# Optimization experiments

Hardware: AMD Instinct MI355X
Metric: run time of the kernel (lower is better)

The kernel has to match this reference:

```python
import jax, jax.numpy as jnp
import numpy as np

NUM_HEADS = 16
LN_EPS = 1e-5

def _gelu(x):
    return jax.nn.gelu(x, approximate=False)  # torch default GELU is exact (erf)

def setup_inputs() -> dict:
    key = jax.random.key(0)
    ks = jax.random.split(key, 12)
    B, S, E = 2, 2048, 1024
    H = E // 2
    s = lambda fan_in: 1.0 / np.sqrt(fan_in)
    inp = {
        "x": jax.random.normal(ks[0], (B, S, E), jnp.float32),
        "Wq": jax.random.normal(ks[1], (E, E), jnp.float32) * s(E),
        "bq": jnp.zeros((E,), jnp.float32),
        "Wk": jax.random.normal(ks[2], (E, E), jnp.float32) * s(E),
        "bk": jnp.zeros((E,), jnp.float32),
        "Wv": jax.random.normal(ks[3], (E, E), jnp.float32) * s(E),
        "bv": jnp.zeros((E,), jnp.float32),
        "Wo": jax.random.normal(ks[4], (E, E), jnp.float32) * s(E),
        "bo": jnp.zeros((E,), jnp.float32),
        "dp_w1": jax.random.normal(ks[5], (E, H), jnp.float32) * s(E),
        "dp_b1": jnp.zeros((H,), jnp.float32),
        "ln_g": jnp.ones((H,), jnp.float32),
        "ln_b": jnp.zeros((H,), jnp.float32),
        "dp_w2": jax.random.normal(ks[6], (H, 1), jnp.float32) * s(H),
        "dp_b2": jnp.zeros((1,), jnp.float32),
        "g_w1": jax.random.normal(ks[7], (1, 16), jnp.float32),
        "g_b1": jnp.zeros((16,), jnp.float32),
        "g_w2": jax.random.normal(ks[8], (16, 1), jnp.float32) * s(16),
        "g_b2": jnp.zeros((1,), jnp.float32),
    }
    return inp


def reference(x, Wq, bq, Wk, bk, Wv, bv, Wo, bo,
              dp_w1, dp_b1, ln_g, ln_b, dp_w2, dp_b2,
              g_w1, g_b1, g_w2, g_b2):
    B, S, E = x.shape
    Hn = NUM_HEADS
    Dh = E // Hn
    scale = Dh ** -0.5

    Q = (x @ Wq + bq).reshape(B, S, Hn, Dh)
    K = (x @ Wk + bk).reshape(B, S, Hn, Dh)
    V = (x @ Wv + bv).reshape(B, S, Hn, Dh)

    # (B, H, q, k)
    logits = jnp.einsum('bqhd,bkhd->bhqk', Q, K) * scale
    causal = jnp.tril(jnp.ones((S, S), bool))
    logits = jnp.where(causal, logits, -jnp.inf)
    attn = jax.nn.softmax(logits, axis=-1)

    # drift probe: Linear -> LayerNorm -> GELU -> Linear, squeeze -> (B, S)
    h = x @ dp_w1 + dp_b1
    mu = h.mean(-1, keepdims=True)
    var = ((h - mu) ** 2).mean(-1, keepdims=True)
    h = (h - mu) / jnp.sqrt(var + LN_EPS) * ln_g + ln_b
    drift = (_gelu(h) @ dp_w2 + dp_b2)[..., 0]

    # drift_to_gate: Linear(1,16) -> GELU -> Linear(16,1) -> Tanh -> (B, S)
    g = _gelu(drift[..., None] * g_w1[0] + g_b1)
    gate = jnp.tanh(g @ g_w2 + g_b2)[..., 0]  # (B, S), indexed by key position

    gated = attn * gate[:, None, None, :]  # dropout p=0 -> identity
    out = jnp.einsum('bhqk,bkhd->bqhd', gated, V).reshape(B, S, E)
    return out @ Wo + bo
```

## Files before the change

### kernel.cpp

```cpp
#include <hip/hip_runtime.h>
#include <math.h>
#include <stdint.h>

#define B_   2
#define S_   2048
#define E_   1024
#define NH   16
#define DH   64
#define HID  512
#define NCAT 3584
#define MTOK 4096

typedef unsigned short ushort_t;
typedef short  s16x8  __attribute__((ext_vector_type(8)));
typedef unsigned short us4 __attribute__((ext_vector_type(4)));
typedef float  f32x4  __attribute__((ext_vector_type(4)));

static constexpr float LN_EPS    = 1e-5f;
static constexpr float SCALE     = 0.125f;
static constexpr float INV_SQRT2 = 0.70710678118654752440f;

__device__ __forceinline__ float gelu_exact(float v) {
    return 0.5f * v * (1.0f + erff(v * INV_SQRT2));
}

__device__ __forceinline__ ushort_t f2bf(float f) {
    unsigned int u = __float_as_uint(f);
    unsigned int r = u + 0x7fffu + ((u >> 16) & 1u);
    return (ushort_t)(r >> 16);
}
__device__ __forceinline__ float bf2f(ushort_t s) {
    return __uint_as_float(((unsigned int)s) << 16);
}

__device__ __forceinline__ void stage16(const void* g, void* ldsbase) {
#if __has_builtin(__builtin_amdgcn_global_load_lds)
    __builtin_amdgcn_global_load_lds(
        (const __attribute__((address_space(1))) void*)g,
        (__attribute__((address_space(3))) void*)ldsbase, 16, 0, 0);
#else
    ((uint4*)ldsbase)[threadIdx.x & 63] = *(const uint4*)g;
#endif
}

__device__ __forceinline__ void xcd_swizzle(int gx, int gy, int& bx, int& by) {
    const int T = gx * gy;
    const int lin = blockIdx.y * gx + blockIdx.x;
    const int work = (lin & 7) * (T >> 3) + (lin >> 3);
    bx = work % gx;
    by = work / gx;
}

__global__ __launch_bounds__(256) void split_kernel(
    const float* __restrict__ src, ushort_t* __restrict__ dh,
    ushort_t* __restrict__ dl, int n4)
{
    int i = blockIdx.x * 256 + threadIdx.x;
    if (i >= n4) return;
    float4 v = ((const float4*)src)[i];
    float vv[4] = {v.x, v.y, v.z, v.w};
    us4 h, l;
    #pragma unroll
    for (int j = 0; j < 4; ++j) {
        ushort_t hh = f2bf(vv[j]);
        h[j] = hh;
        l[j] = f2bf(vv[j] - bf2f(hh));
    }
    *(us4*)&dh[i * 4] = h;
    *(us4*)&dl[i * 4] = l;
}

__global__ __launch_bounds__(256) void transpose_split_kernel(
    const float* __restrict__ W, int N,
    ushort_t* __restrict__ th, ushort_t* __restrict__ tl)
{
    __shared__ float tile[32][33];
    const int k0 = blockIdx.x * 32, n0 = blockIdx.y * 32;
    const int t = threadIdx.x;
    const int r = t >> 3, c4 = (t & 7) * 4;

    float4 v = *(const float4*)&W[(size_t)(k0 + r) * N + n0 + c4];
    tile[r][c4 + 0] = v.x; tile[r][c4 + 1] = v.y;
    tile[r][c4 + 2] = v.z; tile[r][c4 + 3] = v.w;
    __syncthreads();

    us4 h, l;
    #pragma unroll
    for (int i = 0; i < 4; ++i) {
        float x = tile[c4 + i][r];
        ushort_t hh = f2bf(x);
        h[i] = hh;
        l[i] = f2bf(x - bf2f(hh));
    }
    *(us4*)&th[(size_t)(n0 + r) * E_ + k0 + c4] = h;
    *(us4*)&tl[(size_t)(n0 + r) * E_ + k0 + c4] = l;
}

__global__ void concat_bias_kernel(
    const float* __restrict__ bq, const float* __restrict__ bk,
    const float* __restrict__ bv, const float* __restrict__ b1,
    float* __restrict__ bcat)
{
    int i = blockIdx.x * 256 + threadIdx.x;
    if (i >= NCAT) return;
    float v;
    if      (i < 1024) v = bq[i];
    else if (i < 2048) v = bk[i - 1024];
    else if (i < 3072) v = bv[i - 2048];
    else               v = b1[i - 3072];
    bcat[i] = v;
}

struct GemmCtx {
    int lane, w, wr, wc;
};

__device__ __forceinline__ void gemm_core(
    const ushort_t* __restrict__ Ah, const ushort_t* __restrict__ Al,
    const ushort_t* __restrict__ Bh, const ushort_t* __restrict__ Bl,
    int row0, int col0, int Kd,
    ushort_t* Ahs, ushort_t* Als, ushort_t* Bhs, ushort_t* Bls,
    f32x4 (&acc)[4][4], const GemmCtx& cx)
{
    const int lr = cx.lane >> 2;
    const int lc = (cx.lane & 3) * 8;

    for (int k0 = 0; k0 < Kd; k0 += 32) {
        #pragma unroll
        for (int ii = 0; ii < 2; ++ii) {
            const int r0 = (cx.w * 2 + ii) * 16;
            const size_t ga = (size_t)(row0 + r0 + lr) * Kd + k0 + lc;
            const size_t gb = (size_t)(col0 + r0 + lr) * Kd + k0 + lc;
            stage16(Ah + ga, &Ahs[r0 * 32]);
            stage16(Al + ga, &Als[r0 * 32]);
            stage16(Bh + gb, &Bhs[r0 * 32]);
            stage16(Bl + gb, &Bls[r0 * 32]);
        }
        __syncthreads();

        const int rA = cx.wr * 64 + (cx.lane & 15);
        const int rB = cx.wc * 64 + (cx.lane & 15);
        const int kq = (cx.lane >> 4) * 8;
        s16x8 fah[4], fal[4], fbh[4], fbl[4];
        #pragma unroll
        for (int i = 0; i < 4; ++i) {
            fah[i] = *(const s16x8*)&Ahs[(rA + i * 16) * 32 + kq];
            fal[i] = *(const s16x8*)&Als[(rA + i * 16) * 32 + kq];
            fbh[i] = *(const s16x8*)&Bhs[(rB + i * 16) * 32 + kq];
            fbl[i] = *(const s16x8*)&Bls[(rB + i * 16) * 32 + kq];
        }
        __builtin_amdgcn_s_setprio(1);
        #pragma unroll
        for (int i = 0; i < 4; ++i)
            #pragma unroll
            for (int j = 0; j < 4; ++j) {
                acc[i][j] = __builtin_amdgcn_mfma_f32_16x16x32_bf16(fah[i], fbh[j], acc[i][j], 0, 0, 0);
                acc[i][j] = __builtin_amdgcn_mfma_f32_16x16x32_bf16(fah[i], fbl[j], acc[i][j], 0, 0, 0);
                acc[i][j] = __builtin_amdgcn_mfma_f32_16x16x32_bf16(fal[i], fbh[j], acc[i][j], 0, 0, 0);
            }
        __builtin_amdgcn_s_setprio(0);
        __syncthreads();
    }
}

__global__ __launch_bounds__(256) void mfma_gemm_qkvh_kernel(
    const ushort_t* __restrict__ Ah, const ushort_t* __restrict__ Al,
    const ushort_t* __restrict__ Bh, const ushort_t* __restrict__ Bl,
    const float* __restrict__ bias,
    ushort_t* __restrict__ Qh, ushort_t* __restrict__ Ql,
    ushort_t* __restrict__ Kh, ushort_t* __restrict__ Kl,
    float* __restrict__ v32, float* __restrict__ h32)
{
    __shared__ __align__(16) ushort_t Ahs[128 * 32];
    __shared__ __align__(16) ushort_t Als[128 * 32];
    __shared__ __align__(16) ushort_t Bhs[128 * 32];
    __shared__ __align__(16) ushort_t Bls[128 * 32];

    int bx, by;
    xcd_swizzle(28, 32, bx, by);
    const int row0 = by * 128, col0 = bx * 128;

    GemmCtx cx;
    cx.lane = threadIdx.x & 63;
    cx.w    = threadIdx.x >> 6;
    cx.wr   = cx.w >> 1; cx.wc = cx.w & 1;

    f32x4 acc[4][4] = {};
    gemm_core(Ah, Al, Bh, Bl, row0, col0, E_, Ahs, Als, Bhs, Bls, acc, cx);

    const int crow = row0 + cx.wr * 64 + ((cx.lane >> 4) * 4);
    const int ccol0 = col0 + cx.wc * 64 + (cx.lane & 15);

    #pragma unroll
    for (int j = 0; j < 4; ++j) {
        const int gcol = ccol0 + j * 16;
        const float bv = bias[gcol];
        #pragma unroll
        for (int i = 0; i < 4; ++i)
            #pragma unroll
            for (int r = 0; r < 4; ++r) {
                const int row = crow + i * 16 + r;
                float val = acc[i][j][r] + bv;
                if (gcol < 1024) {
                    val *= SCALE;
                    ushort_t hi = f2bf(val);
                    Qh[(size_t)row * 1024 + gcol] = hi;
                    Ql[(size_t)row * 1024 + gcol] = f2bf(val - bf2f(hi));
                } else if (gcol < 2048) {
                    ushort_t hi = f2bf(val);
                    Kh[(size_t)row * 1024 + gcol - 1024] = hi;
                    Kl[(size_t)row * 1024 + gcol - 1024] = f2bf(val - bf2f(hi));
                } else if (gcol < 3072) {
                    v32[(size_t)row * 1024 + gcol - 2048] = val;
                } else {
                    h32[(size_t)row * 512 + gcol - 3072] = val;
                }
            }
    }
}

__global__ __launch_bounds__(256) void mfma_gemm_kernel(
    const ushort_t* __restrict__ Ah, const ushort_t* __restrict__ Al,
    const ushort_t* __restrict__ Bh, const ushort_t* __restrict__ Bl,
    const float* __restrict__ bias,
    float* __restrict__ C, int N, int Kd)
{
    __shared__ __align__(16) ushort_t Ahs[128 * 32];
    __shared__ __align__(16) ushort_t Als[128 * 32];
    __shared__ __align__(16) ushort_t Bhs[128 * 32];
    __shared__ __align__(16) ushort_t Bls[128 * 32];

    int bx, by;
    xcd_swizzle(gridDim.x, gridDim.y, bx, by);
    const int row0 = by * 128, col0 = bx * 128;

    GemmCtx cx;
    cx.lane = threadIdx.x & 63;
    cx.w    = threadIdx.x >> 6;
    cx.wr   = cx.w >> 1; cx.wc = cx.w & 1;

    f32x4 acc[4][4] = {};
    gemm_core(Ah, Al, Bh, Bl, row0, col0, Kd, Ahs, Als, Bhs, Bls, acc, cx);

    const int crow = row0 + cx.wr * 64 + ((cx.lane >> 4) * 4);
    const int ccol = col0 + cx.wc * 64 + (cx.lane & 15);
    #pragma unroll
    for (int j = 0; j < 4; ++j) {
        const float bv = bias[ccol + j * 16];
        #pragma unroll
        for (int i = 0; i < 4; ++i)
            #pragma unroll
            for (int r = 0; r < 4; ++r)
                C[(size_t)(crow + i * 16 + r) * N + ccol + j * 16] = acc[i][j][r] + bv;
    }
}

__global__ __launch_bounds__(256) void ln_gate_kernel(
    const float* __restrict__ h32,
    const float* __restrict__ lng, const float* __restrict__ lnb,
    const float* __restrict__ w2,  const float* __restrict__ b2,
    const float* __restrict__ gw1, const float* __restrict__ gb1,
    const float* __restrict__ gw2, const float* __restrict__ gb2,
    float* __restrict__ gate)
{
    const int row  = blockIdx.x * 4 + (threadIdx.x >> 6);
    const int lane = threadIdx.x & 63;
    const float* h = h32 + (size_t)row * 512;

    float4 a = *(const float4*)&h[lane * 4];
    float4 b = *(const float4*)&h[256 + lane * 4];
    float va[8] = {a.x, a.y, a.z, a.w, b.x, b.y, b.z, b.w};

    float sum = 0.f, sq = 0.f;
    #pragma unroll
    for (int j = 0; j < 8; ++j) { sum += va[j]; sq += va[j] * va[j]; }
    #pragma unroll
    for (int o = 1; o < 64; o <<= 1) {
        sum += __shfl_xor(sum, o);
        sq  += __shfl_xor(sq,  o);
    }
    const float mu  = sum * (1.f / HID);
    const float inv = 1.f / sqrtf(sq * (1.f / HID) - mu * mu + LN_EPS);

    float4 g0 = *(const float4*)&lng[lane * 4];
    float4 g1 = *(const float4*)&lng[256 + lane * 4];
    float4 o0 = *(const float4*)&lnb[lane * 4];
    float4 o1 = *(const float4*)&lnb[256 + lane * 4];
    float4 w0 = *(const float4*)&w2[lane * 4];
    float4 w1 = *(const float4*)&w2[256 + lane * 4];
    float gg[8] = {g0.x, g0.y, g0.z, g0.w, g1.x, g1.y, g1.z, g1.w};
    float bb[8] = {o0.x, o0.y, o0.z, o0.w, o1.x, o1.y, o1.z, o1.w};
    float ww[8] = {w0.x, w0.y, w0.z, w0.w, w1.x, w1.y, w1.z, w1.w};

    float part = 0.f;
    #pragma unroll
    for (int j = 0; j < 8; ++j) {
        float nx = (va[j] - mu) * inv * gg[j] + bb[j];
        part += gelu_exact(nx) * ww[j];
    }
    #pragma unroll
    for (int o = 1; o < 64; o <<= 1) part += __shfl_xor(part, o);

    if (lane == 0) {
        float drift = part + b2[0];
        float gacc = gb2[0];
        #pragma unroll
        for (int i = 0; i < 16; ++i) {
            float t = fmaf(drift, gw1[i], gb1[i]);
            gacc = fmaf(gelu_exact(t), gw2[i], gacc);
        }
        gate[row] = tanhf(gacc);
    }
}

__global__ __launch_bounds__(256) void v_transpose_kernel(
    const float* __restrict__ v32, const float* __restrict__ gate,
    ushort_t* __restrict__ Vth, ushort_t* __restrict__ Vtl)
{
    __shared__ float T[64 * 68];
    const int kt = blockIdx.x, bh = blockIdx.y;
    const int b = bh >> 4, h = bh & 15;
    const int tid = threadIdx.x;

    #pragma unroll
    for (int it = 0; it < 4; ++it) {
        int idx = tid + it * 256;
        int tokr = idx >> 4, f4 = idx & 15;
        int tok = b * S_ + kt * 64 + tokr;
        float g = gate[tok];
        float4 v = *(const float4*)&v32[(size_t)tok * 1024 + h * 64 + f4 * 4];
        T[(f4 * 4 + 0) * 68 + tokr] = v.x * g;
        T[(f4 * 4 + 1) * 68 + tokr] = v.y * g;
        T[(f4 * 4 + 2) * 68 + tokr] = v.z * g;
        T[(f4 * 4 + 3) * 68 + tokr] = v.w * g;
    }
    __syncthreads();

    const int d = tid >> 2, t0 = (tid & 3) * 16;
    const size_t obase = (size_t)bh * 64 * S_ + (size_t)d * S_ + kt * 64 + t0;
    s16x8 h8[2], l8[2];
    #pragma unroll
    for (int u = 0; u < 16; ++u) {
        float f = T[d * 68 + t0 + u];
        ushort_t hh = f2bf(f);
        h8[u >> 3][u & 7] = (short)hh;
        l8[u >> 3][u & 7] = (short)f2bf(f - bf2f(hh));
    }
    *(s16x8*)&Vth[obase]     = h8[0];
    *(s16x8*)&Vth[obase + 8] = h8[1];
    *(s16x8*)&Vtl[obase]     = l8[0];
    *(s16x8*)&Vtl[obase + 8] = l8[1];
}

__global__ __launch_bounds__(512, 4) void attn_mfma_kernel(
    const ushort_t* __restrict__ Qh, const ushort_t* __restrict__ Ql,
    const ushort_t* __restrict__ Kh, const ushort_t* __restrict__ Kl,
    const ushort_t* __restrict__ Vth, const ushort_t* __restrict__ Vtl,
    ushort_t* __restrict__ ch, ushort_t* __restrict__ cl)
{
    __shared__ __align__(16) ushort_t smem[36864];
    ushort_t* const Qhs = smem;
    ushort_t* const Qls = smem + 9216;
    ushort_t* const Khs = smem + 18432;
    ushort_t* const Kls = smem + 23040;
    ushort_t* const Vhs = smem + 27648;
    ushort_t* const Vls = smem + 32256;
    unsigned int* const Ps = (unsigned int*)smem;

    const int tid  = threadIdx.x;
    const int lane = tid & 63;
    const int w    = tid >> 6;
    const int g    = lane >> 4;
    const int c    = lane & 15;

    const int lin  = blockIdx.y * 16 + blockIdx.x;
    const int work = (lin & 7) * 64 + (lin >> 3);
    const int bh   = work >> 4;
    const int qt   = 15 - (work & 15);
    const int b    = bh >> 4, h = bh & 15;
    const int q0   = qt * 128;

    const size_t qkb = (size_t)b * S_ * 1024 + h * 64;
    const size_t vtb = (size_t)bh * 64 * S_;

    #pragma unroll
    for (int it = 0; it < 2; ++it) {
        int c2 = tid + it * 512;
        int row = c2 >> 3, sl = c2 & 7;
        s16x8 vh = *(const s16x8*)&Qh[qkb + (size_t)(q0 + row) * 1024 + sl * 8];
        s16x8 vl = *(const s16x8*)&Ql[qkb + (size_t)(q0 + row) * 1024 + sl * 8];
        *(s16x8*)&Qhs[row * 72 + sl * 8] = vh;
        *(s16x8*)&Qls[row * 72 + sl * 8] = vl;
    }

    f32x4 o4[4] = {};
    float m[4], l[4];
    #pragma unroll
    for (int r = 0; r < 4; ++r) { m[r] = -INFINITY; l[r] = 0.f; }

    const int pbase = w * (16 * 68);
    __syncthreads();

    s16x8 qfh[2], qfl[2];
    #pragma unroll
    for (int ks = 0; ks < 2; ++ks) {
        qfh[ks] = *(const s16x8*)&Qhs[(w * 16 + c) * 72 + ks * 32 + g * 8];
        qfl[ks] = *(const s16x8*)&Qls[(w * 16 + c) * 72 + ks * 32 + g * 8];
    }

    const int srow = tid >> 3, ssl = tid & 7;

    s16x8 pkh, pkl, pvh, pvl;
    pkh = *(const s16x8*)&Kh [qkb + (size_t)srow * 1024 + ssl * 8];
    pkl = *(const s16x8*)&Kl [qkb + (size_t)srow * 1024 + ssl * 8];
    pvh = *(const s16x8*)&Vth[vtb + (size_t)srow * S_ + ssl * 8];
    pvl = *(const s16x8*)&Vtl[vtb + (size_t)srow * S_ + ssl * 8];

    const int ktmax = 2 * qt + 1;
    const int qwave = q0 + w * 16;

    for (int kt = 0; kt <= ktmax; ++kt) {
        const int k0 = kt * 64;
        *(s16x8*)&Khs[srow * 72 + ssl * 8] = pkh;
        *(s16x8*)&Kls[srow * 72 + ssl * 8] = pkl;
        *(s16x8*)&Vhs[srow * 72 + ssl * 8] = pvh;
        *(s16x8*)&Vls[srow * 72 + ssl * 8] = pvl;
        __syncthreads();

        if (kt < ktmax) {
            const int kn = k0 + 64;
            pkh = *(const s16x8*)&Kh [qkb + (size_t)(kn + srow) * 1024 + ssl * 8];
            pkl = *(const s16x8*)&Kl [qkb + (size_t)(kn + srow) * 1024 + ssl * 8];
            pvh = *(const s16x8*)&Vth[vtb + (size_t)srow * S_ + kn + ssl * 8];
            pvl = *(const s16x8*)&Vtl[vtb + (size_t)srow * S_ + kn + ssl * 8];
        }

        if (k0 <= qwave + 15) {
            f32x4 s4[4] = {};
            __builtin_amdgcn_s_setprio(1);
            #pragma unroll
            for (int j = 0; j < 4; ++j)
                #pragma unroll
                for (int ks = 0; ks < 2; ++ks) {
                    s16x8 kfh = *(const s16x8*)&Khs[(c + j * 16) * 72 + ks * 32 + g * 8];
                    s16x8 kfl = *(const s16x8*)&Kls[(c + j * 16) * 72 + ks * 32 + g * 8];
                    s4[j] = __builtin_amdgcn_mfma_f32_16x16x32_bf16(qfh[ks], kfh, s4[j], 0, 0, 0);
                    s4[j] = __builtin_amdgcn_mfma_f32_16x16x32_bf16(qfh[ks], kfl, s4[j], 0, 0, 0);
                    s4[j] = __builtin_amdgcn_mfma_f32_16x16x32_bf16(qfl[ks], kfh, s4[j], 0, 0, 0);
                }
            __builtin_amdgcn_s_setprio(0);

            if (k0 + 63 > qwave) {
                #pragma unroll
                for (int j = 0; j < 4; ++j)
                    #pragma unroll
                    for (int r = 0; r < 4; ++r)
                        if (k0 + c + j * 16 > qwave + g * 4 + r)
                            s4[j][r] = -INFINITY;
            }

            #pragma unroll
            for (int r = 0; r < 4; ++r) {
                float mx = fmaxf(fmaxf(s4[0][r], s4[1][r]), fmaxf(s4[2][r], s4[3][r]));
                #pragma unroll
                for (int o = 1; o < 16; o <<= 1) mx = fmaxf(mx, __shfl_xor(mx, o));
                float mn = fmaxf(m[r], mx);
                float corr = (m[r] == -INFINITY) ? 0.f : __expf(m[r] - mn);
                float ps = 0.f;
                #pragma unroll
                for (int j = 0; j < 4; ++j) {
                    float p = __expf(s4[j][r] - mn);
                    s4[j][r] = p;
                    ps += p;
                }
                #pragma unroll
                for (int o = 1; o < 16; o <<= 1) ps += __shfl_xor(ps, o);
                l[r] = l[r] * corr + ps;
                m[r] = mn;
                #pragma unroll
                for (int j = 0; j < 4; ++j) o4[j][r] *= corr;
            }

            #pragma unroll
            for (int j = 0; j < 4; ++j)
                #pragma unroll
                for (int r = 0; r < 4; ++r) {
                    float p = s4[j][r];
                    ushort_t hi = f2bf(p);
                    ushort_t lo = f2bf(p - bf2f(hi));
                    Ps[pbase + (g * 4 + r) * 68 + c + j * 16] =
                        (unsigned int)hi | ((unsigned int)lo << 16);
                }
            asm volatile("s_waitcnt lgkmcnt(0)" ::: "memory");
            __builtin_amdgcn_sched_barrier(0);

            s16x8 pah[2], pal[2];
            #pragma unroll
            for (int ks = 0; ks < 2; ++ks) {
                uint4 a = *(const uint4*)&Ps[pbase + c * 68 + ks * 32 + g * 8];
                uint4 bq = *(const uint4*)&Ps[pbase + c * 68 + ks * 32 + g * 8 + 4];
                unsigned int wd[8] = {a.x, a.y, a.z, a.w, bq.x, bq.y, bq.z, bq.w};
                union { unsigned int u[4]; s16x8 v; } uh, ul;
                #pragma unroll
                for (int t = 0; t < 4; ++t) {
                    uh.u[t] = (wd[2 * t] & 0xffffu) | (wd[2 * t + 1] << 16);
                    ul.u[t] = (wd[2 * t] >> 16) | (wd[2 * t + 1] & 0xffff0000u);
                }
                pah[ks] = uh.v;
                pal[ks] = ul.v;
            }

            __builtin_amdgcn_s_setprio(1);
            #pragma unroll
            for (int j = 0; j < 4; ++j)
                #pragma unroll
                for (int ks = 0; ks < 2; ++ks) {
                    s16x8 vfh = *(const s16x8*)&Vhs[(c + j * 16) * 72 + ks * 32 + g * 8];
                    s16x8 vfl = *(const s16x8*)&Vls[(c + j * 16) * 72 + ks * 32 + g * 8];
                    o4[j] = __builtin_amdgcn_mfma_f32_16x16x32_bf16(pah[ks], vfh, o4[j], 0, 0, 0);
                    o4[j] = __builtin_amdgcn_mfma_f32_16x16x32_bf16(pah[ks], vfl, o4[j], 0, 0, 0);
                    o4[j] = __builtin_amdgcn_mfma_f32_16x16x32_bf16(pal[ks], vfh, o4[j], 0, 0, 0);
                }
            __builtin_amdgcn_s_setprio(0);
        }
        __syncthreads();
    }

    float inv[4];
    #pragma unroll
    for (int r = 0; r < 4; ++r) inv[r] = 1.f / l[r];
    #pragma unroll
    for (int j = 0; j < 4; ++j)
        #pragma unroll
        for (int r = 0; r < 4; ++r) {
            float val = o4[j][r] * inv[r];
            int tok = b * S_ + q0 + w * 16 + g * 4 + r;
            int col = h * 64 + c + j * 16;
            ushort_t hi = f2bf(val);
            ch[(size_t)tok * 1024 + col] = hi;
            cl[(size_t)tok * 1024 + col] = f2bf(val - bf2f(hi));
        }
}

extern "C" void kernel_launch(void* const* d_in, const int* in_sizes, int n_in,
                              void* d_out, int out_size, void* d_ws, size_t ws_size,
                              hipStream_t stream)
{
    const float* x    = (const float*)d_in[0];
    const float* Wq   = (const float*)d_in[1];  const float* bq   = (const float*)d_in[2];
    const float* Wk   = (const float*)d_in[3];  const float* bk   = (const float*)d_in[4];
    const float* Wv   = (const float*)d_in[5];  const float* bv   = (const float*)d_in[6];
    const float* Wo   = (const float*)d_in[7];  const float* bo   = (const float*)d_in[8];
    const float* dpw1 = (const float*)d_in[9];  const float* dpb1 = (const float*)d_in[10];
    const float* lng  = (const float*)d_in[11]; const float* lnb  = (const float*)d_in[12];
    const float* dpw2 = (const float*)d_in[13]; const float* dpb2 = (const float*)d_in[14];
    const float* gw1  = (const float*)d_in[15]; const float* gb1  = (const float*)d_in[16];
    const float* gw2  = (const float*)d_in[17]; const float* gb2  = (const float*)d_in[18];
    float* out = (float*)d_out;

    float* ws   = (float*)d_ws;
    float* v32  = ws;
    float* h32  = v32 + (size_t)MTOK * E_;
    float* bcat = h32 + (size_t)MTOK * HID;
    float* gate = bcat + NCAT;
    ushort_t* bp   = (ushort_t*)(gate + MTOK);
    ushort_t* xh   = bp;
    ushort_t* xl   = xh  + (size_t)MTOK * E_;
    ushort_t* bth  = xl  + (size_t)MTOK * E_;
    ushort_t* btl  = bth + (size_t)NCAT * E_;
    ushort_t* woth = btl + (size_t)NCAT * E_;
    ushort_t* wotl = woth + (size_t)E_ * E_;
    ushort_t* Qhb  = wotl + (size_t)E_ * E_;
    ushort_t* Qlb  = Qhb + (size_t)MTOK * E_;
    ushort_t* Khb  = Qlb + (size_t)MTOK * E_;
    ushort_t* Klb  = Khb + (size_t)MTOK * E_;
    ushort_t* Vthb = Klb + (size_t)MTOK * E_;
    ushort_t* Vtlb = Vthb + (size_t)MTOK * E_;
    ushort_t* chb  = xh;
    ushort_t* clb  = xl;

    hipLaunchKernelGGL(split_kernel, dim3(4096), dim3(256), 0, stream,
                       x, xh, xl, MTOK * E_ / 4);
    hipLaunchKernelGGL(transpose_split_kernel, dim3(32, 32), dim3(256), 0, stream,
                       Wq, E_, bth, btl);
    hipLaunchKernelGGL(transpose_split_kernel, dim3(32, 32), dim3(256), 0, stream,
                       Wk, E_, bth + (size_t)1024 * E_, btl + (size_t)1024 * E_);
    hipLaunchKernelGGL(transpose_split_kernel, dim3(32, 32), dim3(256), 0, stream,
                       Wv, E_, bth + (size_t)2048 * E_, btl + (size_t)2048 * E_);
    hipLaunchKernelGGL(transpose_split_kernel, dim3(32, 16), dim3(256), 0, stream,
                       dpw1, HID, bth + (size_t)3072 * E_, btl + (size_t)3072 * E_);
    hipLaunchKernelGGL(transpose_split_kernel, dim3(32, 32), dim3(256), 0, stream,
                       Wo, E_, woth, wotl);
    hipLaunchKernelGGL(concat_bias_kernel, dim3(14), dim3(256), 0, stream,
                       bq, bk, bv, dpb1, bcat);

    hipLaunchKernelGGL(mfma_gemm_qkvh_kernel, dim3(28, 32), dim3(256), 0, stream,
                       xh, xl, bth, btl, bcat, Qhb, Qlb, Khb, Klb, v32, h32);

    hipLaunchKernelGGL(ln_gate_kernel, dim3(MTOK / 4), dim3(256), 0, stream,
                       h32, lng, lnb, dpw2, dpb2, gw1, gb1, gw2, gb2, gate);
    hipLaunchKernelGGL(v_transpose_kernel, dim3(32, 32), dim3(256), 0, stream,
                       v32, gate, Vthb, Vtlb);

    hipLaunchKernelGGL(attn_mfma_kernel, dim3(S_ / 128, B_ * NH), dim3(512), 0, stream,
                       Qhb, Qlb, Khb, Klb, Vthb, Vtlb, chb, clb);

    hipLaunchKernelGGL(mfma_gemm_kernel, dim3(E_ / 128, MTOK / 128), dim3(256), 0, stream,
                       chb, clb, woth, wotl, bo, out, E_, E_);
}
```

Before: 447.2 us.

## Merge preprocessing kernels and restructure attention softmax with transposed score MFMA

Fuses the split, five weight transpose-splits and bias concat launches into one preprocessing kernel, removing launch overhead. In the attention kernel, Q fragments are loaded straight from global memory instead of staged through LDS. The score MFMA operands are swapped so each lane owns one query row, which turns per-row shuffle reductions into two cross-group shuffles. It also skips the rescale when the running max does not change, and writes P as packed hi/lo bf16 into separate swizzled LDS arrays using v_cvt_pk_bf16_f32. These changes cut shuffles and repacking but add ds_bpermute calls and more complex indexing.

Measured after the change: 396.2 us. -11.4%, faster.

```diff
diff --git a/kernel.cpp b/kernel.cpp
--- a/kernel.cpp
+++ b/kernel.cpp
@@ -51,57 +51,70 @@
     by = work / gx;
 }
 
-__global__ __launch_bounds__(256) void split_kernel(
-    const float* __restrict__ src, ushort_t* __restrict__ dh,
-    ushort_t* __restrict__ dl, int n4)
-{
-    int i = blockIdx.x * 256 + threadIdx.x;
-    if (i >= n4) return;
-    float4 v = ((const float4*)src)[i];
-    float vv[4] = {v.x, v.y, v.z, v.w};
-    us4 h, l;
-    #pragma unroll
-    for (int j = 0; j < 4; ++j) {
-        ushort_t hh = f2bf(vv[j]);
-        h[j] = hh;
-        l[j] = f2bf(vv[j] - bf2f(hh));
-    }
-    *(us4*)&dh[i * 4] = h;
-    *(us4*)&dl[i * 4] = l;
-}
-
-__global__ __launch_bounds__(256) void transpose_split_kernel(
-    const float* __restrict__ W, int N,
-    ushort_t* __restrict__ th, ushort_t* __restrict__ tl)
-{
-    __shared__ float tile[32][33];
-    const int k0 = blockIdx.x * 32, n0 = blockIdx.y * 32;
-    const int t = threadIdx.x;
-    const int r = t >> 3, c4 = (t & 7) * 4;
-
-    float4 v = *(const float4*)&W[(size_t)(k0 + r) * N + n0 + c4];
-    tile[r][c4 + 0] = v.x; tile[r][c4 + 1] = v.y;
-    tile[r][c4 + 2] = v.z; tile[r][c4 + 3] = v.w;
-    __syncthreads();
-
-    us4 h, l;
-    #pragma unroll
-    for (int i = 0; i < 4; ++i) {
-        float x = tile[c4 + i][r];
-        ushort_t hh = f2bf(x);
-        h[i] = hh;
-        l[i] = f2bf(x - bf2f(hh));
-    }
-    *(us4*)&th[(size_t)(n0 + r) * E_ + k0 + c4] = h;
-    *(us4*)&tl[(size_t)(n0 + r) * E_ + k0 + c4] = l;
-}
-
-__global__ void concat_bias_kernel(
+__global__ __launch_bounds__(256) void preproc_kernel(
+    const float* __restrict__ x,
+    const float* __restrict__ Wq, const float* __restrict__ Wk,
+    const float* __restrict__ Wv, const float* __restrict__ Wo,
+    const float* __restrict__ dpw1,
     const float* __restrict__ bq, const float* __restrict__ bk,
     const float* __restrict__ bv, const float* __restrict__ b1,
+    ushort_t* __restrict__ xh, ushort_t* __restrict__ xl,
+    ushort_t* __restrict__ bth, ushort_t* __restrict__ btl,
+    ushort_t* __restrict__ woth, ushort_t* __restrict__ wotl,
     float* __restrict__ bcat)
 {
-    int i = blockIdx.x * 256 + threadIdx.x;
+    __shared__ float tile[32][33];
+    int bid = blockIdx.x;
+    const int t = threadIdx.x;
+
+    if (bid < 1024) {
+        int base = bid * 1024 + t;
+        #pragma unroll
+        for (int it = 0; it < 4; ++it) {
+            int i = base + it * 256;
+            float4 v = ((const float4*)x)[i];
+            float vv[4] = {v.x, v.y, v.z, v.w};
+            us4 h, l;
+            #pragma unroll
+            for (int j = 0; j < 4; ++j) {
+                ushort_t hh = f2bf(vv[j]);
+                h[j] = hh;
+                l[j] = f2bf(vv[j] - bf2f(hh));
+            }
+            *(us4*)&xh[(size_t)i * 4] = h;
+            *(us4*)&xl[(size_t)i * 4] = l;
+        }
+        return;
+    }
+    bid -= 1024;
+    if (bid < 4608) {
+        const float* W; ushort_t *th, *tl; int N, kx, ny;
+        if (bid < 1024)      { W = Wq;   th = bth;                        tl = btl;                        N = 1024; kx = bid & 31; ny = bid >> 5; }
+        else if (bid < 2048) { W = Wk;   th = bth + (size_t)1024 * E_;    tl = btl + (size_t)1024 * E_;    N = 1024; kx = (bid - 1024) & 31; ny = (bid - 1024) >> 5; }
+        else if (bid < 3072) { W = Wv;   th = bth + (size_t)2048 * E_;    tl = btl + (size_t)2048 * E_;    N = 1024; kx = (bid - 2048) & 31; ny = (bid - 2048) >> 5; }
+        else if (bid < 4096) { W = Wo;   th = woth;                       tl = wotl;                       N = 1024; kx = (bid - 3072) & 31; ny = (bid - 3072) >> 5; }
+        else                 { W = dpw1; th = bth + (size_t)3072 * E_;    tl = btl + (size_t)3072 * E_;    N = 512;  kx = (bid - 4096) & 31; ny = (bid - 4096) >> 5; }
+
+        const int k0 = kx * 32, n0 = ny * 32;
+        const int r = t >> 3, c4 = (t & 7) * 4;
+        float4 v = *(const float4*)&W[(size_t)(k0 + r) * N + n0 + c4];
+        tile[r][c4 + 0] = v.x; tile[r][c4 + 1] = v.y;
+        tile[r][c4 + 2] = v.z; tile[r][c4 + 3] = v.w;
+        __syncthreads();
+        us4 h, l;
+        #pragma unroll
+        for (int i = 0; i < 4; ++i) {
+            float xv = tile[c4 + i][r];
+            ushort_t hh = f2bf(xv);
+            h[i] = hh;
+            l[i] = f2bf(xv - bf2f(hh));
+        }
+        *(us4*)&th[(size_t)(n0 + r) * E_ + k0 + c4] = h;
+        *(us4*)&tl[(size_t)(n0 + r) * E_ + k0 + c4] = l;
+        return;
+    }
+    bid -= 4608;
+    int i = bid * 256 + t;
     if (i >= NCAT) return;
     float v;
     if      (i < 1024) v = bq[i];
@@ -306,8 +319,8 @@
         float gacc = gb2[0];
         #pragma unroll
         for (int i = 0; i < 16; ++i) {
-            float t = fmaf(drift, gw1[i], gb1[i]);
-            gacc = fmaf(gelu_exact(t), gw2[i], gacc);
+            float tt = fmaf(drift, gw1[i], gb1[i]);
+            gacc = fmaf(gelu_exact(tt), gw2[i], gacc);
         }
         gate[row] = tanhf(gacc);
     }
@@ -358,14 +371,10 @@
     const ushort_t* __restrict__ Vth, const ushort_t* __restrict__ Vtl,
     ushort_t* __restrict__ ch, ushort_t* __restrict__ cl)
 {
-    __shared__ __align__(16) ushort_t smem[36864];
-    ushort_t* const Qhs = smem;
-    ushort_t* const Qls = smem + 9216;
-    ushort_t* const Khs = smem + 18432;
-    ushort_t* const Kls = smem + 23040;
-    ushort_t* const Vhs = smem + 27648;
-    ushort_t* const Vls = smem + 32256;
-    unsigned int* const Ps = (unsigned int*)smem;
+    __shared__ __align__(16) ushort_t Khs[64 * 72], Kls[64 * 72];
+    __shared__ __align__(16) ushort_t Vhs[64 * 72], Vls[64 * 72];
+    __shared__ __align__(16) unsigned int Ph[8 * 16 * 32];
+    __shared__ __align__(16) unsigned int Pl[8 * 16 * 32];
 
     const int tid  = threadIdx.x;
     const int lane = tid & 63;
@@ -383,30 +392,19 @@
     const size_t qkb = (size_t)b * S_ * 1024 + h * 64;
     const size_t vtb = (size_t)bh * 64 * S_;
 
-    #pragma unroll
-    for (int it = 0; it < 2; ++it) {
-        int c2 = tid + it * 512;
-        int row = c2 >> 3, sl = c2 & 7;
-        s16x8 vh = *(const s16x8*)&Qh[qkb + (size_t)(q0 + row) * 1024 + sl * 8];
-        s16x8 vl = *(const s16x8*)&Ql[qkb + (size_t)(q0 + row) * 1024 + sl * 8];
-        *(s16x8*)&Qhs[row * 72 + sl * 8] = vh;
-        *(s16x8*)&Qls[row * 72 + sl * 8] = vl;
-    }
+    const int qwave = q0 + w * 16;
+
+    const size_t qrow = qkb + (size_t)(qwave + c) * 1024;
+    s16x8 qfh[2], qfl[2];
+    qfh[0] = *(const s16x8*)&Qh[qrow + g * 8];
+    qfh[1] = *(const s16x8*)&Qh[qrow + 32 + g * 8];
+    qfl[0] = *(const s16x8*)&Ql[qrow + g * 8];
+    qfl[1] = *(const s16x8*)&Ql[qrow + 32 + g * 8];
 
     f32x4 o4[4] = {};
-    float m[4], l[4];
-    #pragma unroll
-    for (int r = 0; r < 4; ++r) { m[r] = -INFINITY; l[r] = 0.f; }
-
-    const int pbase = w * (16 * 68);
-    __syncthreads();
-
-    s16x8 qfh[2], qfl[2];
-    #pragma unroll
-    for (int ks = 0; ks < 2; ++ks) {
-        qfh[ks] = *(const s16x8*)&Qhs[(w * 16 + c) * 72 + ks * 32 + g * 8];
-        qfl[ks] = *(const s16x8*)&Qls[(w * 16 + c) * 72 + ks * 32 + g * 8];
-    }
+    float m = -INFINITY, l = 0.f;
+
+    #define PIDX(c_, kp_) ((w << 9) + ((c_) << 5) + ((kp_) ^ (((c_) & 7) << 2)))
 
     const int srow = tid >> 3, ssl = tid & 7;
 
@@ -417,7 +415,6 @@
     pvl = *(const s16x8*)&Vtl[vtb + (size_t)srow * S_ + ssl * 8];
 
     const int ktmax = 2 * qt + 1;
-    const int qwave = q0 + w * 16;
 
     for (int kt = 0; kt <= ktmax; ++kt) {
         const int k0 = kt * 64;
@@ -444,9 +441,9 @@
                 for (int ks = 0; ks < 2; ++ks) {
                     s16x8 kfh = *(const s16x8*)&Khs[(c + j * 16) * 72 + ks * 32 + g * 8];
                     s16x8 kfl = *(const s16x8*)&Kls[(c + j * 16) * 72 + ks * 32 + g * 8];
-                    s4[j] = __builtin_amdgcn_mfma_f32_16x16x32_bf16(qfh[ks], kfh, s4[j], 0, 0, 0);
-                    s4[j] = __builtin_amdgcn_mfma_f32_16x16x32_bf16(qfh[ks], kfl, s4[j], 0, 0, 0);
-                    s4[j] = __builtin_amdgcn_mfma_f32_16x16x32_bf16(qfl[ks], kfh, s4[j], 0, 0, 0);
+                    s4[j] = __builtin_amdgcn_mfma_f32_16x16x32_bf16(kfh, qfh[ks], s4[j], 0, 0, 0);
+                    s4[j] = __builtin_amdgcn_mfma_f32_16x16x32_bf16(kfh, qfl[ks], s4[j], 0, 0, 0);
+                    s4[j] = __builtin_amdgcn_mfma_f32_16x16x32_bf16(kfl, qfh[ks], s4[j], 0, 0, 0);
                 }
             __builtin_amdgcn_s_setprio(0);
 
@@ -455,59 +452,79 @@
                 for (int j = 0; j < 4; ++j)
                     #pragma unroll
                     for (int r = 0; r < 4; ++r)
-                        if (k0 + c + j * 16 > qwave + g * 4 + r)
+                        if (k0 + j * 16 + g * 4 + r > qwave + c)
                             s4[j][r] = -INFINITY;
             }
 
-            #pragma unroll
-            for (int r = 0; r < 4; ++r) {
-                float mx = fmaxf(fmaxf(s4[0][r], s4[1][r]), fmaxf(s4[2][r], s4[3][r]));
+            float pmax = -INFINITY;
+            #pragma unroll
+            for (int j = 0; j < 4; ++j)
                 #pragma unroll
-                for (int o = 1; o < 16; o <<= 1) mx = fmaxf(mx, __shfl_xor(mx, o));
-                float mn = fmaxf(m[r], mx);
-                float corr = (m[r] == -INFINITY) ? 0.f : __expf(m[r] - mn);
-                float ps = 0.f;
+                for (int r = 0; r < 4; ++r) pmax = fmaxf(pmax, s4[j][r]);
+            pmax = fmaxf(pmax, __shfl_xor(pmax, 16));
+            pmax = fmaxf(pmax, __shfl_xor(pmax, 32));
+
+            const bool nomax = __all(pmax <= m);
+            const float mn = nomax ? m : fmaxf(m, pmax);
+
+            float ps = 0.f;
+            #pragma unroll
+            for (int j = 0; j < 4; ++j)
                 #pragma unroll
-                for (int j = 0; j < 4; ++j) {
+                for (int r = 0; r < 4; ++r) {
                     float p = __expf(s4[j][r] - mn);
                     s4[j][r] = p;
                     ps += p;
                 }
+            ps += __shfl_xor(ps, 16);
+            ps += __shfl_xor(ps, 32);
+
+            if (nomax) {
+                l += ps;
+            } else {
+                float corr = (m == -INFINITY) ? 0.f : __expf(m - mn);
+                l = l * corr + ps;
+                m = mn;
                 #pragma unroll
-                for (int o = 1; o < 16; o <<= 1) ps += __shfl_xor(ps, o);
-                l[r] = l[r] * corr + ps;
-                m[r] = mn;
-                #pragma unroll
-                for (int j = 0; j < 4; ++j) o4[j][r] *= corr;
+                for (int r = 0; r < 4; ++r) {
+                    int src = ((g << 4) | (g * 4 + r)) << 2;
+                    float cr = __int_as_float(
+                        __builtin_amdgcn_ds_bpermute(src, __float_as_int(corr)));
+                    #pragma unroll
+                    for (int j = 0; j < 4; ++j) o4[j][r] *= cr;
+                }
             }
 
             #pragma unroll
             for (int j = 0; j < 4; ++j)
                 #pragma unroll
-                for (int r = 0; r < 4; ++r) {
-                    float p = s4[j][r];
-                    ushort_t hi = f2bf(p);
-                    ushort_t lo = f2bf(p - bf2f(hi));
-                    Ps[pbase + (g * 4 + r) * 68 + c + j * 16] =
-                        (unsigned int)hi | ((unsigned int)lo << 16);
+                for (int p = 0; p < 2; ++p) {
+                    float e  = s4[j][2 * p];
+                    float od = s4[j][2 * p + 1];
+                    unsigned int hi2, lo2;
+                    asm volatile("v_cvt_pk_bf16_f32 %0, %1, %2"
+                                 : "=v"(hi2) : "v"(e), "v"(od));
+                    float ef = __uint_as_float(hi2 << 16);
+                    float of = __uint_as_float(hi2 & 0xffff0000u);
+                    float el = e - ef, ol = od - of;
+                    asm volatile("v_cvt_pk_bf16_f32 %0, %1, %2"
+                                 : "=v"(lo2) : "v"(el), "v"(ol));
+                    const int kp = j * 8 + g * 2 + p;
+                    Ph[PIDX(c, kp)] = hi2;
+                    Pl[PIDX(c, kp)] = lo2;
                 }
             asm volatile("s_waitcnt lgkmcnt(0)" ::: "memory");
             __builtin_amdgcn_sched_barrier(0);
 
+            union U4 { uint4 u; s16x8 v; };
             s16x8 pah[2], pal[2];
             #pragma unroll
             for (int ks = 0; ks < 2; ++ks) {
-                uint4 a = *(const uint4*)&Ps[pbase + c * 68 + ks * 32 + g * 8];
-                uint4 bq = *(const uint4*)&Ps[pbase + c * 68 + ks * 32 + g * 8 + 4];
-                unsigned int wd[8] = {a.x, a.y, a.z, a.w, bq.x, bq.y, bq.z, bq.w};
-                union { unsigned int u[4]; s16x8 v; } uh, ul;
-                #pragma unroll
-                for (int t = 0; t < 4; ++t) {
-                    uh.u[t] = (wd[2 * t] & 0xffffu) | (wd[2 * t + 1] << 16);
-                    ul.u[t] = (wd[2 * t] >> 16) | (wd[2 * t + 1] & 0xffff0000u);
-                }
-                pah[ks] = uh.v;
-                pal[ks] = ul.v;
+                U4 a, bb;
+                a.u  = *(const uint4*)&Ph[PIDX(c, ks * 16 + g * 4)];
+                bb.u = *(const uint4*)&Pl[PIDX(c, ks * 16 + g * 4)];
+                pah[ks] = a.v;
+                pal[ks] = bb.v;
             }
 
             __builtin_amdgcn_s_setprio(1);
@@ -528,18 +545,24 @@
 
     float inv[4];
     #pragma unroll
-    for (int r = 0; r < 4; ++r) inv[r] = 1.f / l[r];
+    for (int r = 0; r < 4; ++r) {
+        int src = ((g << 4) | (g * 4 + r)) << 2;
+        float lb = __int_as_float(
+            __builtin_amdgcn_ds_bpermute(src, __float_as_int(l)));
+        inv[r] = 1.f / lb;
+    }
     #pragma unroll
     for (int j = 0; j < 4; ++j)
         #pragma unroll
         for (int r = 0; r < 4; ++r) {
             float val = o4[j][r] * inv[r];
-            int tok = b * S_ + q0 + w * 16 + g * 4 + r;
+            int tok = b * S_ + qwave + g * 4 + r;
             int col = h * 64 + c + j * 16;
             ushort_t hi = f2bf(val);
             ch[(size_t)tok * 1024 + col] = hi;
             cl[(size_t)tok * 1024 + col] = f2bf(val - bf2f(hi));
         }
+    #undef PIDX
 }
 
 extern "C" void kernel_launch(void* const* d_in, const int* in_sizes, int n_in,
@@ -579,20 +602,9 @@
     ushort_t* chb  = xh;
     ushort_t* clb  = xl;
 
-    hipLaunchKernelGGL(split_kernel, dim3(4096), dim3(256), 0, stream,
-                       x, xh, xl, MTOK * E_ / 4);
-    hipLaunchKernelGGL(transpose_split_kernel, dim3(32, 32), dim3(256), 0, stream,
-                       Wq, E_, bth, btl);
-    hipLaunchKernelGGL(transpose_split_kernel, dim3(32, 32), dim3(256), 0, stream,
-                       Wk, E_, bth + (size_t)1024 * E_, btl + (size_t)1024 * E_);
-    hipLaunchKernelGGL(transpose_split_kernel, dim3(32, 32), dim3(256), 0, stream,
-                       Wv, E_, bth + (size_t)2048 * E_, btl + (size_t)2048 * E_);
-    hipLaunchKernelGGL(transpose_split_kernel, dim3(32, 16), dim3(256), 0, stream,
-                       dpw1, HID, bth + (size_t)3072 * E_, btl + (size_t)3072 * E_);
-    hipLaunchKernelGGL(transpose_split_kernel, dim3(32, 32), dim3(256), 0, stream,
-                       Wo, E_, woth, wotl);
-    hipLaunchKernelGGL(concat_bias_kernel, dim3(14), dim3(256), 0, stream,
-                       bq, bk, bv, dpb1, bcat);
+    hipLaunchKernelGGL(preproc_kernel, dim3(5646), dim3(256), 0, stream,
+                       x, Wq, Wk, Wv, Wo, dpw1, bq, bk, bv, dpb1,
+                       xh, xl, bth, btl, woth, wotl, bcat);
 
     hipLaunchKernelGGL(mfma_gemm_qkvh_kernel, dim3(28, 32), dim3(256), 0, stream,
                        xh, xl, bth, btl, bcat, Qhb, Qlb, Khb, Klb, v32, h32);
```
